# Performance work log

Measured on AMD Instinct MI355X. Metric: run time of the kernel, lower is better.

Reference implementation:

```python
import jax, jax.numpy as jnp
import numpy as np

B, D, H, DH, L = 2, 1024, 16, 64, 4
FF = 4 * D
COUNTS = (512, 256, 128, 64, 16)  # seq, local_seq, scattering, expression, fusion
EPS = 1e-5


def layer_norm(x, gamma):
    mu = jnp.mean(x, axis=-1, keepdims=True)
    var = jnp.mean((x - mu) ** 2, axis=-1, keepdims=True)
    return (x - mu) * jax.lax.rsqrt(var + EPS) * gamma


def build_zorro_mask(counts):
    # faithful to the torch code, including the `|` / `==` precedence quirk:
    # zorro_mask_fusion = (zorro_mask | tf) == FUSION(4)
    types = jnp.concatenate([jnp.full((c,), i, dtype=jnp.int32) for i, c in enumerate(counts)])
    tf, tt = types[:, None], types[None, :]
    m0 = tf == tt
    fusion_rows = (m0.astype(jnp.int32) | tf) == 4
    mask = m0 | fusion_rows
    S = int(sum(counts))
    nf = counts[4]
    exp_rows = (types == 3)[:, None]
    col_ok = (jnp.arange(S) < (S - nf))[None, :]
    return mask | (exp_rows & col_ok)


def setup_inputs() -> dict:
    key = jax.random.key(0)
    ks = jax.random.split(key, 13)
    s = 0.02
    inp = {
        "rna_tokens": jax.random.normal(ks[0], (B, COUNTS[0], D), jnp.float32),
        "roi_tokens": jax.random.normal(ks[1], (B, COUNTS[1], D), jnp.float32),
        "structure_tokens": jax.random.normal(ks[2], (B, COUNTS[2], D), jnp.float32),
        "expression_tokens": jax.random.normal(ks[3], (B, COUNTS[3], D), jnp.float32),
        "fusion_tokens": jax.random.normal(ks[4], (B, COUNTS[4], D), jnp.float32),
        "qw": jax.random.normal(ks[5], (L, D, H * DH), jnp.float32) * s,
        "kvw": jax.random.normal(ks[6], (L, D, 2 * H * DH), jnp.float32) * s,
        "ow": jax.random.normal(ks[7], (L, H * DH, D), jnp.float32) * s,
        "ag": jnp.ones((L, D), jnp.float32),
        "fg": jnp.ones((L, D), jnp.float32),
        "w1": jax.random.normal(ks[8], (L, D, FF), jnp.float32) * s,
        "w2": jax.random.normal(ks[9], (L, FF, D), jnp.float32) * s,
        "gamma": jnp.ones((D,), jnp.float32),
    }
    return inp


def reference(rna_tokens, roi_tokens, structure_tokens, expression_tokens, fusion_tokens,
              qw, kvw, ow, ag, fg, w1, w2, gamma):
    streams = (rna_tokens, roi_tokens, structure_tokens, expression_tokens, fusion_tokens)
    counts = tuple(t.shape[1] for t in streams)
    tokens = jnp.concatenate(streams, axis=1)  # [B, S, D]
    b, S, d = tokens.shape
    mask = build_zorro_mask(counts)  # [S, S] bool
    scale = DH ** -0.5
    neg = jnp.finfo(tokens.dtype).min
    attn_list = []
    for l in range(L):
        x = layer_norm(tokens, ag[l])
        q = (x @ qw[l]).reshape(b, S, H, DH)
        kv = x @ kvw[l]
        k = kv[..., : H * DH].reshape(b, S, H, DH)
        v = kv[..., H * DH:].reshape(b, S, H, DH)
        sim = jnp.einsum('bihd,bjhd->bhij', q, k) * scale
        sim = jnp.where(mask, sim, neg)
        attn = jax.nn.softmax(sim, axis=-1)  # [B, H, S, S]
        attn_list.append(attn)
        out = jnp.einsum('bhij,bjhd->bihd', attn, v).reshape(b, S, H * DH) @ ow[l]
        tokens = out + tokens
        y = layer_norm(tokens, fg[l])
        tokens = jax.nn.gelu(y @ w1[l], approximate=False) @ w2[l] + tokens
    tokens = layer_norm(tokens, gamma)
    splits = np.cumsum(counts)[:-1].tolist()
    seq_t, local_t, scat_t, exp_t, fus_t = jnp.split(tokens, splits, axis=1)
    return (seq_t, local_t, scat_t, exp_t, fus_t, jnp.stack(attn_list))
```

## Files before the change

kernel.cpp:

```cpp
#include <hip/hip_runtime.h>
#include <math.h>
#include <stdint.h>

typedef __bf16 bf16;
typedef __attribute__((ext_vector_type(8))) bf16 bf16x8;
typedef __attribute__((ext_vector_type(4))) bf16 bf16x4;
typedef __attribute__((ext_vector_type(4))) float f4;

__device__ __forceinline__ f4 mfma(bf16x8 a, bf16x8 b, f4 c){
  return __builtin_amdgcn_mfma_f32_16x16x32_bf16(a, b, c, 0, 0, 0);
}

static constexpr int S_TOT = 976;
static constexpr int MR = 1952;
static constexpr int MRP = 2048;
static constexpr size_t ATT_BASE = 1998848;
static constexpr size_t ATT_L = 30482432;

__device__ __forceinline__ void gload16(const void* g, const void* l){
  __builtin_amdgcn_global_load_lds(
      (const __attribute__((address_space(1))) void*)(uintptr_t)g,
      (__attribute__((address_space(3))) void*)(uint32_t)(uintptr_t)l,
      16, 0, 0);
}

__device__ __forceinline__ unsigned pk2(float a, float b){
  unsigned short ua = __builtin_bit_cast(unsigned short, (bf16)a);
  unsigned short ub = __builtin_bit_cast(unsigned short, (bf16)b);
  return ((unsigned)ub << 16) | (unsigned)ua;
}

__global__ __launch_bounds__(256) void k_concat(const float* __restrict__ r0, const float* __restrict__ r1,
                                                const float* __restrict__ r2, const float* __restrict__ r3,
                                                const float* __restrict__ r4, float* __restrict__ tok){
  int idx = blockIdx.x*256 + threadIdx.x;
  if (idx >= MR*256) return;
  int d4 = idx & 255;
  int row = idx >> 8;
  int b = row / S_TOT, s = row % S_TOT;
  const float* src; int off;
  if (s < 512)      { src = r0; off = b*512 + s; }
  else if (s < 768) { src = r1; off = b*256 + (s-512); }
  else if (s < 896) { src = r2; off = b*128 + (s-768); }
  else if (s < 960) { src = r3; off = b*64  + (s-896); }
  else              { src = r4; off = b*16  + (s-960); }
  ((f4*)tok)[idx] = ((const f4*)src)[off*256 + d4];
}

__global__ __launch_bounds__(256) void k_ln_bf(const float* __restrict__ in, const float* __restrict__ g,
                                               bf16* __restrict__ out){
  int wid = threadIdx.x >> 6, lane = threadIdx.x & 63;
  int row = blockIdx.x*4 + wid;
  const float* p = in + (size_t)row*1024;
  f4 v[4];
#pragma unroll
  for (int i=0;i<4;i++) v[i] = ((const f4*)p)[i*64 + lane];
  float sum=0.f, sq=0.f;
#pragma unroll
  for (int i=0;i<4;i++){
#pragma unroll
    for (int c=0;c<4;c++){ float x=v[i][c]; sum+=x; sq+=x*x; } }
#pragma unroll
  for (int d=1; d<64; d<<=1){ sum += __shfl_xor(sum,d); sq += __shfl_xor(sq,d); }
  float mu = sum*(1.f/1024.f);
  float var = sq*(1.f/1024.f) - mu*mu;
  float rs = rsqrtf(var + 1e-5f);
#pragma unroll
  for (int i=0;i<4;i++){
    f4 gg = ((const f4*)g)[i*64 + lane];
    bf16x4 o;
#pragma unroll
    for (int c=0;c<4;c++) o[c] = (bf16)((v[i][c]-mu)*rs*gg[c]);
    *(bf16x4*)&out[(size_t)row*1024 + (size_t)(i*64+lane)*4] = o;
  }
}

__global__ __launch_bounds__(256) void k_ln_out(const float* __restrict__ in, const float* __restrict__ g,
                                                float* __restrict__ out){
  int wid = threadIdx.x >> 6, lane = threadIdx.x & 63;
  int row = blockIdx.x*4 + wid;
  int b = row / S_TOT, s = row % S_TOT;
  size_t dst;
  if (s < 512)      dst = (size_t)(b*512 + s)*1024;
  else if (s < 768) dst = 1048576 + (size_t)(b*256 + (s-512))*1024;
  else if (s < 896) dst = 1572864 + (size_t)(b*128 + (s-768))*1024;
  else if (s < 960) dst = 1835008 + (size_t)(b*64  + (s-896))*1024;
  else              dst = 1966080 + (size_t)(b*16  + (s-960))*1024;
  const float* p = in + (size_t)row*1024;
  f4 v[4];
#pragma unroll
  for (int i=0;i<4;i++) v[i] = ((const f4*)p)[i*64 + lane];
  float sum=0.f, sq=0.f;
#pragma unroll
  for (int i=0;i<4;i++){
#pragma unroll
    for (int c=0;c<4;c++){ float x=v[i][c]; sum+=x; sq+=x*x; } }
#pragma unroll
  for (int d=1; d<64; d<<=1){ sum += __shfl_xor(sum,d); sq += __shfl_xor(sq,d); }
  float mu = sum*(1.f/1024.f);
  float var = sq*(1.f/1024.f) - mu*mu;
  float rs = rsqrtf(var + 1e-5f);
#pragma unroll
  for (int i=0;i<4;i++){
    f4 gg = ((const f4*)g)[i*64 + lane];
    f4 o;
#pragma unroll
    for (int c=0;c<4;c++) o[c] = (v[i][c]-mu)*rs*gg[c];
    ((f4*)(out + dst))[i*64 + lane] = o;
  }
}

__global__ __launch_bounds__(256) void k_wtransz(const float* __restrict__ src, int ldsrc, int coloff, long srcZ,
                                                 bf16* __restrict__ dst, int K, long dstZ){
  src += (size_t)blockIdx.z*srcZ;
  dst += (size_t)blockIdx.z*dstZ;
  __shared__ float t[32][33];
  int kb = blockIdx.x*32, nb = blockIdx.y*32;
  int tx = threadIdx.x & 31, ty = threadIdx.x >> 5;
#pragma unroll
  for (int i=0;i<32;i+=8) t[ty+i][tx] = src[(size_t)(kb+ty+i)*ldsrc + coloff + nb + tx];
  __syncthreads();
#pragma unroll
  for (int i=0;i<32;i+=8) dst[(size_t)(nb+ty+i)*K + kb + tx] = (bf16)t[tx][ty+i];
}

__global__ __launch_bounds__(256) void k_attn_pv(const bf16* __restrict__ q, const bf16* __restrict__ k,
                                                 const bf16* __restrict__ vT, int ld,
                                                 float* __restrict__ aout, bf16* __restrict__ O){
  int z = blockIdx.y; int b = z >> 4, h = z & 15;
  int wid = threadIdx.x >> 6, lane = threadIdx.x & 63;
  int r0 = (blockIdx.x*4 + wid)*16;
  if (r0 >= S_TOT) return;
  int cs, ce;
  if (r0 < 512)      { cs = 0;   ce = 512; }
  else if (r0 < 768) { cs = 512; ce = 768; }
  else if (r0 < 896) { cs = 768; ce = 896; }
  else if (r0 < 960) { cs = 0;   ce = 960; }
  else               { cs = 0;   ce = 976; }
  int lm = lane & 15, lg = lane >> 4;
  const float scale = 0.125f;
  const bf16* qp = q + (size_t)(b*S_TOT + r0 + lm)*ld + h*64 + lg*8;
  bf16x8 qf0 = *(const bf16x8*)qp;
  bf16x8 qf1 = *(const bf16x8*)(qp + 32);
  const bf16* kbase = k + (size_t)b*S_TOT*ld + h*64 + lg*8;
  const bf16* vbase = vT + (size_t)z*64*S_TOT;
  int nfull = (ce - cs) & ~31;
  bool tail = ((ce - cs) & 16) != 0;
  float m = -1e30f, s = 0.f;
  for (int cb = cs; cb < cs + nfull; cb += 32){
    const bf16* kp = kbase + (size_t)(cb + lm)*ld;
    bf16x8 k00 = *(const bf16x8*)kp;
    bf16x8 k01 = *(const bf16x8*)(kp + 32);
    const bf16* kp2 = kp + (size_t)16*ld;
    bf16x8 k10 = *(const bf16x8*)kp2;
    bf16x8 k11 = *(const bf16x8*)(kp2 + 32);
    f4 c0 = {0.f,0.f,0.f,0.f}, c1 = {0.f,0.f,0.f,0.f};
    c0 = mfma(k00, qf0, c0); c0 = mfma(k01, qf1, c0);
    c1 = mfma(k10, qf0, c1); c1 = mfma(k11, qf1, c1);
    float vm = m;
#pragma unroll
    for (int r=0;r<4;r++) vm = fmaxf(vm, fmaxf(c0[r]*scale, c1[r]*scale));
    float e = 0.f;
#pragma unroll
    for (int r=0;r<4;r++) e += __expf(c0[r]*scale - vm) + __expf(c1[r]*scale - vm);
    s = s*__expf(m - vm) + e;
    m = vm;
  }
  if (tail){
    int cb = cs + nfull;
    const bf16* kp = kbase + (size_t)(cb + lm)*ld;
    bf16x8 k00 = *(const bf16x8*)kp;
    bf16x8 k01 = *(const bf16x8*)(kp + 32);
    f4 c0 = {0.f,0.f,0.f,0.f};
    c0 = mfma(k00, qf0, c0); c0 = mfma(k01, qf1, c0);
    float vm = m;
#pragma unroll
    for (int r=0;r<4;r++) vm = fmaxf(vm, c0[r]*scale);
    float e = 0.f;
#pragma unroll
    for (int r=0;r<4;r++) e += __expf(c0[r]*scale - vm);
    s = s*__expf(m - vm) + e;
    m = vm;
  }
#pragma unroll
  for (int d=16; d<64; d<<=1){
    float om = __shfl_xor(m, d), os = __shfl_xor(s, d);
    float nm = fmaxf(m, om);
    s = s*__expf(m - nm) + os*__expf(om - nm);
    m = nm;
  }
  float inv = 1.f / s;
  float* orow = aout + (size_t)z*S_TOT*S_TOT + (size_t)(r0 + lm)*S_TOT;
  f4 acc[4];
#pragma unroll
  for (int nf=0;nf<4;nf++){ f4 zf = {0.f,0.f,0.f,0.f}; acc[nf] = zf; }
  bool msel = (lg >= 2);
  int srcA = lm + ((lg & 1) << 5);
  int srcB = srcA + 16;
  auto step = [&](int cb, bool has2){
    const bf16* kp = kbase + (size_t)(cb + lm)*ld;
    bf16x8 k00 = *(const bf16x8*)kp;
    bf16x8 k01 = *(const bf16x8*)(kp + 32);
    f4 c0 = {0.f,0.f,0.f,0.f}, c1 = {0.f,0.f,0.f,0.f};
    c0 = mfma(k00, qf0, c0); c0 = mfma(k01, qf1, c0);
    if (has2){
      const bf16* kp2 = kp + (size_t)16*ld;
      bf16x8 k10 = *(const bf16x8*)kp2;
      bf16x8 k11 = *(const bf16x8*)(kp2 + 32);
      c1 = mfma(k10, qf0, c1); c1 = mfma(k11, qf1, c1);
    }
    f4 p0, p1;
#pragma unroll
    for (int r=0;r<4;r++) p0[r] = __expf(c0[r]*scale - m)*inv;
#pragma unroll
    for (int r=0;r<4;r++) p1[r] = has2 ? __expf(c1[r]*scale - m)*inv : 0.f;
    *(f4*)(orow + cb + lg*4) = p0;
    if (has2) *(f4*)(orow + cb + 16 + lg*4) = p1;
    unsigned lo0 = pk2(p0[0], p0[1]), hi0 = pk2(p0[2], p0[3]);
    unsigned lo1 = pk2(p1[0], p1[1]), hi1 = pk2(p1[2], p1[3]);
    unsigned a0 = __shfl(lo0, srcA), a1 = __shfl(lo1, srcA);
    unsigned b0 = __shfl(hi0, srcA), b1 = __shfl(hi1, srcA);
    unsigned c0s = __shfl(lo0, srcB), c1s = __shfl(lo1, srcB);
    unsigned d0 = __shfl(hi0, srcB), d1 = __shfl(hi1, srcB);
    union { unsigned u[4]; bf16x8 v; } pu;
    pu.u[0] = msel ? a1 : a0;
    pu.u[1] = msel ? b1 : b0;
    pu.u[2] = msel ? c1s : c0s;
    pu.u[3] = msel ? d1 : d0;
    bf16x8 pa = pu.v;
#pragma unroll
    for (int nf=0;nf<4;nf++){
      bf16x8 vf = *(const bf16x8*)(vbase + (size_t)(nf*16 + lm)*S_TOT + cb + lg*8);
      acc[nf] = mfma(pa, vf, acc[nf]);
    }
  };
  for (int cb = cs; cb < cs + nfull; cb += 32) step(cb, true);
  if (tail) step(cs + nfull, false);
  bf16* obase = O + (size_t)(b*S_TOT + r0)*1024 + h*64;
#pragma unroll
  for (int nf=0;nf<4;nf++)
#pragma unroll
    for (int r=0;r<4;r++)
      obase[(size_t)(lg*4 + r)*1024 + nf*16 + lm] = (bf16)acc[nf][r];
  float* zrow = aout + (size_t)z*S_TOT*S_TOT + (size_t)r0*S_TOT;
  int cs4 = cs >> 2, ce4 = ce >> 2;
  for (int r2=0;r2<16;r2++){
    f4* rb = (f4*)(zrow + (size_t)r2*S_TOT);
    f4 zf = {0.f,0.f,0.f,0.f};
    for (int c4 = lane; c4 < cs4; c4 += 64)        rb[c4] = zf;
    for (int c4 = ce4 + lane; c4 < 244; c4 += 64)  rb[c4] = zf;
  }
}

template<int BM, bool OUTBF, bool RESID, bool GELU, bool VT>
__global__ __launch_bounds__(256) void k_gemm2(
    const bf16* __restrict__ A, int lda,
    const bf16* __restrict__ Bw, int ldb,
    float* __restrict__ Cf, bf16* __restrict__ Cb, int ldc,
    const float* __restrict__ R, bf16* __restrict__ vTout, int M, int N, int K)
{
  constexpr int MF = BM/32;
  __shared__ bf16 As[2][BM*32];
  __shared__ bf16 Bs[2][128*32];
  int tid = threadIdx.x, lane = tid & 63, wid = tid >> 6;
  int lm = lane & 15, lg = lane >> 4;
  int wr = (wid >> 1)*(BM/2), wc = (wid & 1)*64;
  int mb = blockIdx.x*BM, nb = blockIdx.y*128;
  f4 acc[MF][4];
#pragma unroll
  for (int i=0;i<MF;i++)
#pragma unroll
    for (int j=0;j<4;j++){ f4 zf = {0.f,0.f,0.f,0.f}; acc[i][j] = zf; }
  const bf16* Ab = A + (size_t)mb*lda;
  const bf16* Bb = Bw + (size_t)nb*ldb;
  auto stage = [&](int kt, int buf){
    int k0 = kt*32;
#pragma unroll
    for (int it=0; it<BM/64; it++){
      int cb = it*256 + wid*64;
      int c  = cb + lane;
      gload16(Ab + (size_t)(c>>2)*lda + k0 + (c&3)*8, (char*)As[buf] + cb*16);
    }
#pragma unroll
    for (int it=0; it<2; it++){
      int cb = it*256 + wid*64;
      int c  = cb + lane;
      gload16(Bb + (size_t)(c>>2)*ldb + k0 + (c&3)*8, (char*)Bs[buf] + cb*16);
    }
  };
  stage(0, 0);
  __syncthreads();
  int nkt = K/32;
  for (int kt=0; kt<nkt; kt++){
    int cur = kt & 1;
    if (kt+1 < nkt) stage(kt+1, cur^1);
    bf16x8 af[MF], bfr[4];
#pragma unroll
    for (int mf=0; mf<MF; mf++) af[mf] = *(bf16x8*)&As[cur][(wr + mf*16 + lm)*32 + lg*8];
#pragma unroll
    for (int nf=0; nf<4; nf++)  bfr[nf] = *(bf16x8*)&Bs[cur][(wc + nf*16 + lm)*32 + lg*8];
#pragma unroll
    for (int mf=0; mf<MF; mf++)
#pragma unroll
      for (int nf=0; nf<4; nf++)
        acc[mf][nf] = mfma(af[mf], bfr[nf], acc[mf][nf]);
    __syncthreads();
  }
#pragma unroll
  for (int mf=0; mf<MF; mf++)
#pragma unroll
    for (int nf=0; nf<4; nf++)
#pragma unroll
      for (int r=0; r<4; r++){
        int row = mb + wr + mf*16 + lg*4 + r;
        if (row < M){
          int col = nb + wc + nf*16 + lm;
          float vv = acc[mf][nf][r];
          if (RESID) vv += R[(size_t)row*ldc + col];
          if (GELU)  vv = 0.5f*vv*(1.f + erff(vv*0.70710678f));
          if (OUTBF) Cb[(size_t)row*ldc + col] = (bf16)vv;
          else       Cf[(size_t)row*ldc + col] = vv;
          if (VT && nb >= 2048){
            int cc = col - 2048;
            int hh = cc >> 6, dd = cc & 63;
            int bb = (row >= S_TOT) ? 1 : 0;
            int ss = row - bb*S_TOT;
            vTout[((size_t)((bb<<4) + hh)*64 + dd)*S_TOT + ss] = (bf16)vv;
          }
        }
      }
}

extern "C" void kernel_launch(void* const* d_in, const int* in_sizes, int n_in,
                              void* d_out, int out_size, void* d_ws, size_t ws_size,
                              hipStream_t stream) {
  const float* rna  = (const float*)d_in[0];
  const float* roi  = (const float*)d_in[1];
  const float* stru = (const float*)d_in[2];
  const float* expr = (const float*)d_in[3];
  const float* fus  = (const float*)d_in[4];
  const float* qw   = (const float*)d_in[5];
  const float* kvw  = (const float*)d_in[6];
  const float* ow   = (const float*)d_in[7];
  const float* ag   = (const float*)d_in[8];
  const float* fg   = (const float*)d_in[9];
  const float* w1   = (const float*)d_in[10];
  const float* w2   = (const float*)d_in[11];
  const float* gamma= (const float*)d_in[12];
  float* out = (float*)d_out;

  char* wsb = (char*)d_ws;
  size_t off = 0;
  auto alc = [&](size_t n)->char*{ char* p = wsb + off; off = (off + n + 255) & ~(size_t)255; return p; };
  float* tokens = (float*)alc((size_t)MRP*1024*4);
  bf16* xb    = (bf16*)alc((size_t)MRP*1024*2);
  bf16* qkv   = (bf16*)alc((size_t)MRP*3072*2);
  bf16* vT    = (bf16*)alc((size_t)32*64*S_TOT*2);
  bf16* attno = (bf16*)alc((size_t)MRP*1024*2);
  bf16* hb    = (bf16*)alc((size_t)MRP*4096*2);
  bf16* wqkvT = (bf16*)alc((size_t)4*3072*1024*2);
  bf16* woT   = (bf16*)alc((size_t)4*1024*1024*2);
  bf16* w1T   = (bf16*)alc((size_t)4*4096*1024*2);
  bf16* w2T   = (bf16*)alc((size_t)4*4096*1024*2);
  if (off > ws_size) return;

  k_concat<<<MR, 256, 0, stream>>>(rna, roi, stru, expr, fus, tokens);

  k_wtransz<<<dim3(32,32,4),  256, 0, stream>>>(qw,  1024, 0,    1048576, wqkvT,             1024, 3145728);
  k_wtransz<<<dim3(32,32,4),  256, 0, stream>>>(kvw, 2048, 0,    2097152, wqkvT + 1024*1024, 1024, 3145728);
  k_wtransz<<<dim3(32,32,4),  256, 0, stream>>>(kvw, 2048, 1024, 2097152, wqkvT + 2048*1024, 1024, 3145728);
  k_wtransz<<<dim3(32,32,4),  256, 0, stream>>>(ow,  1024, 0,    1048576, woT, 1024, 1048576);
  k_wtransz<<<dim3(32,128,4), 256, 0, stream>>>(w1,  4096, 0,    4194304, w1T, 1024, 4194304);
  k_wtransz<<<dim3(128,32,4), 256, 0, stream>>>(w2,  1024, 0,    4194304, w2T, 4096, 4194304);

  for (int l=0; l<4; l++){
    k_ln_bf<<<MR/4, 256, 0, stream>>>(tokens, ag + l*1024, xb);

    k_gemm2<128,true,false,false,true><<<dim3(16,24), 256, 0, stream>>>(
        xb, 1024, wqkvT + (size_t)l*3145728, 1024, nullptr, qkv, 3072, nullptr, vT, MR, 3072, 1024);

    float* attL = out + ATT_BASE + (size_t)l*ATT_L;
    k_attn_pv<<<dim3(16,32), 256, 0, stream>>>(qkv, qkv + 1024, vT, 3072, attL, attno);

    k_gemm2<64,false,true,false,false><<<dim3(31,8), 256, 0, stream>>>(
        attno, 1024, woT + (size_t)l*1048576, 1024, tokens, nullptr, 1024, tokens, nullptr, MR, 1024, 1024);

    k_ln_bf<<<MR/4, 256, 0, stream>>>(tokens, fg + l*1024, xb);

    k_gemm2<128,true,false,true,false><<<dim3(16,32), 256, 0, stream>>>(
        xb, 1024, w1T + (size_t)l*4194304, 1024, nullptr, hb, 4096, nullptr, nullptr, MR, 4096, 1024);
    k_gemm2<64,false,true,false,false><<<dim3(31,8), 256, 0, stream>>>(
        hb, 4096, w2T + (size_t)l*4194304, 4096, tokens, nullptr, 1024, tokens, nullptr, MR, 1024, 4096);
  }

  k_ln_out<<<MR/4, 256, 0, stream>>>(tokens, gamma, out);
}
```

Measured before the change: 1.184 ms.

## Split-K the FFN down-projection, fuse residual reduction with next LayerNorm, separate V transpose

The FFN down-projection GEMM now splits K=4096 into two halves across blockIdx.z and uses 128-row tiles, writing fp32 partials to a new workspace buffer. A new kernel sums both partials with the residual and, when another layer follows, also computes the next attention LayerNorm, which removes a separate LN launch. The V transpose moves out of the QKV GEMM epilogue into a dedicated LDS-tiled transpose kernel, and s_setprio hints are placed around the MFMA blocks in the attention kernel. The split-K path adds extra fp32 partial traffic and one more launch per layer in exchange for more blocks on the narrow N=1024 GEMM.

```diff
diff --git a/kernel.cpp b/kernel.cpp
--- a/kernel.cpp
+++ b/kernel.cpp
@@ -75,6 +75,42 @@
   }
 }
 
+template<bool LN>
+__global__ __launch_bounds__(256) void k_red_ln(const float* __restrict__ pA, float* __restrict__ tokens,
+                                                const float* __restrict__ g, bf16* __restrict__ xb){
+  int wid = threadIdx.x >> 6, lane = threadIdx.x & 63;
+  int row = blockIdx.x*4 + wid;
+  const float* p0 = pA + (size_t)row*1024;
+  const float* p1 = pA + (size_t)MRP*1024 + (size_t)row*1024;
+  float* tp = tokens + (size_t)row*1024;
+  f4 v[4];
+  float sum=0.f, sq=0.f;
+#pragma unroll
+  for (int i=0;i<4;i++){
+    f4 a = ((const f4*)p0)[i*64 + lane];
+    f4 b = ((const f4*)p1)[i*64 + lane];
+    f4 t = ((const f4*)tp)[i*64 + lane];
+#pragma unroll
+    for (int c=0;c<4;c++){ float x = t[c] + a[c] + b[c]; v[i][c] = x; if (LN){ sum += x; sq += x*x; } }
+    ((f4*)tp)[i*64 + lane] = v[i];
+  }
+  if (LN){
+#pragma unroll
+    for (int d=1; d<64; d<<=1){ sum += __shfl_xor(sum,d); sq += __shfl_xor(sq,d); }
+    float mu = sum*(1.f/1024.f);
+    float var = sq*(1.f/1024.f) - mu*mu;
+    float rs = rsqrtf(var + 1e-5f);
+#pragma unroll
+    for (int i=0;i<4;i++){
+      f4 gg = ((const f4*)g)[i*64 + lane];
+      bf16x4 o;
+#pragma unroll
+      for (int c=0;c<4;c++) o[c] = (bf16)((v[i][c]-mu)*rs*gg[c]);
+      *(bf16x4*)&xb[(size_t)row*1024 + (size_t)(i*64+lane)*4] = o;
+    }
+  }
+}
+
 __global__ __launch_bounds__(256) void k_ln_out(const float* __restrict__ in, const float* __restrict__ g,
                                                 float* __restrict__ out){
   int wid = threadIdx.x >> 6, lane = threadIdx.x & 63;
@@ -122,6 +158,24 @@
   __syncthreads();
 #pragma unroll
   for (int i=0;i<32;i+=8) dst[(size_t)(nb+ty+i)*K + kb + tx] = (bf16)t[tx][ty+i];
+}
+
+__global__ __launch_bounds__(256) void k_vtrans(const bf16* __restrict__ v, int ld, bf16* __restrict__ vT){
+  int z = blockIdx.y; int b = z >> 4, h = z & 15;
+  int sb = blockIdx.x*64;
+  __shared__ bf16 t[64][72];
+  int tx = threadIdx.x & 63, ty = threadIdx.x >> 6;
+#pragma unroll
+  for (int i=0;i<64;i+=4){
+    int s = sb + ty + i;
+    t[ty+i][tx] = (s < S_TOT) ? v[(size_t)(b*S_TOT + s)*ld + h*64 + tx] : (bf16)0.f;
+  }
+  __syncthreads();
+#pragma unroll
+  for (int i=0;i<64;i+=4){
+    int s = sb + tx;
+    if (s < S_TOT) vT[(size_t)z*64*S_TOT + (size_t)(ty+i)*S_TOT + s] = t[tx][ty+i];
+  }
 }
 
 __global__ __launch_bounds__(256) void k_attn_pv(const bf16* __restrict__ q, const bf16* __restrict__ k,
@@ -155,8 +209,10 @@
     bf16x8 k10 = *(const bf16x8*)kp2;
     bf16x8 k11 = *(const bf16x8*)(kp2 + 32);
     f4 c0 = {0.f,0.f,0.f,0.f}, c1 = {0.f,0.f,0.f,0.f};
+    __builtin_amdgcn_s_setprio(1);
     c0 = mfma(k00, qf0, c0); c0 = mfma(k01, qf1, c0);
     c1 = mfma(k10, qf0, c1); c1 = mfma(k11, qf1, c1);
+    __builtin_amdgcn_s_setprio(0);
     float vm = m;
 #pragma unroll
     for (int r=0;r<4;r++) vm = fmaxf(vm, fmaxf(c0[r]*scale, c1[r]*scale));
@@ -202,6 +258,7 @@
     bf16x8 k00 = *(const bf16x8*)kp;
     bf16x8 k01 = *(const bf16x8*)(kp + 32);
     f4 c0 = {0.f,0.f,0.f,0.f}, c1 = {0.f,0.f,0.f,0.f};
+    __builtin_amdgcn_s_setprio(1);
     c0 = mfma(k00, qf0, c0); c0 = mfma(k01, qf1, c0);
     if (has2){
       const bf16* kp2 = kp + (size_t)16*ld;
@@ -209,6 +266,7 @@
       bf16x8 k11 = *(const bf16x8*)(kp2 + 32);
       c1 = mfma(k10, qf0, c1); c1 = mfma(k11, qf1, c1);
     }
+    __builtin_amdgcn_s_setprio(0);
     f4 p0, p1;
 #pragma unroll
     for (int r=0;r<4;r++) p0[r] = __expf(c0[r]*scale - m)*inv;
@@ -228,11 +286,13 @@
     pu.u[2] = msel ? c1s : c0s;
     pu.u[3] = msel ? d1 : d0;
     bf16x8 pa = pu.v;
+    __builtin_amdgcn_s_setprio(1);
 #pragma unroll
     for (int nf=0;nf<4;nf++){
       bf16x8 vf = *(const bf16x8*)(vbase + (size_t)(nf*16 + lm)*S_TOT + cb + lg*8);
       acc[nf] = mfma(pa, vf, acc[nf]);
     }
+    __builtin_amdgcn_s_setprio(0);
   };
   for (int cb = cs; cb < cs + nfull; cb += 32) step(cb, true);
   if (tail) step(cs + nfull, false);
@@ -252,12 +312,12 @@
   }
 }
 
-template<int BM, bool OUTBF, bool RESID, bool GELU, bool VT>
+template<int BM, bool OUTBF, bool RESID, bool GELU>
 __global__ __launch_bounds__(256) void k_gemm2(
     const bf16* __restrict__ A, int lda,
     const bf16* __restrict__ Bw, int ldb,
     float* __restrict__ Cf, bf16* __restrict__ Cb, int ldc,
-    const float* __restrict__ R, bf16* __restrict__ vTout, int M, int N, int K)
+    const float* __restrict__ R, int M, int N, int K, int kz, long cz)
 {
   constexpr int MF = BM/32;
   __shared__ bf16 As[2][BM*32];
@@ -266,13 +326,14 @@
   int lm = lane & 15, lg = lane >> 4;
   int wr = (wid >> 1)*(BM/2), wc = (wid & 1)*64;
   int mb = blockIdx.x*BM, nb = blockIdx.y*128;
+  int bz = blockIdx.z;
   f4 acc[MF][4];
 #pragma unroll
   for (int i=0;i<MF;i++)
 #pragma unroll
     for (int j=0;j<4;j++){ f4 zf = {0.f,0.f,0.f,0.f}; acc[i][j] = zf; }
-  const bf16* Ab = A + (size_t)mb*lda;
-  const bf16* Bb = Bw + (size_t)nb*ldb;
+  const bf16* Ab = A + (size_t)mb*lda + (size_t)bz*kz;
+  const bf16* Bb = Bw + (size_t)nb*ldb + (size_t)bz*kz;
   auto stage = [&](int kt, int buf){
     int k0 = kt*32;
 #pragma unroll
@@ -319,14 +380,7 @@
           if (RESID) vv += R[(size_t)row*ldc + col];
           if (GELU)  vv = 0.5f*vv*(1.f + erff(vv*0.70710678f));
           if (OUTBF) Cb[(size_t)row*ldc + col] = (bf16)vv;
-          else       Cf[(size_t)row*ldc + col] = vv;
-          if (VT && nb >= 2048){
-            int cc = col - 2048;
-            int hh = cc >> 6, dd = cc & 63;
-            int bb = (row >= S_TOT) ? 1 : 0;
-            int ss = row - bb*S_TOT;
-            vTout[((size_t)((bb<<4) + hh)*64 + dd)*S_TOT + ss] = (bf16)vv;
-          }
+          else       Cf[(size_t)bz*cz + (size_t)row*ldc + col] = vv;
         }
       }
 }
@@ -353,6 +407,7 @@
   size_t off = 0;
   auto alc = [&](size_t n)->char*{ char* p = wsb + off; off = (off + n + 255) & ~(size_t)255; return p; };
   float* tokens = (float*)alc((size_t)MRP*1024*4);
+  float* pA    = (float*)alc((size_t)2*MRP*1024*4);
   bf16* xb    = (bf16*)alc((size_t)MRP*1024*2);
   bf16* qkv   = (bf16*)alc((size_t)MRP*3072*2);
   bf16* vT    = (bf16*)alc((size_t)32*64*S_TOT*2);
@@ -373,24 +428,31 @@
   k_wtransz<<<dim3(32,128,4), 256, 0, stream>>>(w1,  4096, 0,    4194304, w1T, 1024, 4194304);
   k_wtransz<<<dim3(128,32,4), 256, 0, stream>>>(w2,  1024, 0,    4194304, w2T, 4096, 4194304);
 
+  k_ln_bf<<<MR/4, 256, 0, stream>>>(tokens, ag, xb);
+
   for (int l=0; l<4; l++){
-    k_ln_bf<<<MR/4, 256, 0, stream>>>(tokens, ag + l*1024, xb);
-
-    k_gemm2<128,true,false,false,true><<<dim3(16,24), 256, 0, stream>>>(
-        xb, 1024, wqkvT + (size_t)l*3145728, 1024, nullptr, qkv, 3072, nullptr, vT, MR, 3072, 1024);
+    k_gemm2<128,true,false,false><<<dim3(16,24), 256, 0, stream>>>(
+        xb, 1024, wqkvT + (size_t)l*3145728, 1024, nullptr, qkv, 3072, nullptr, MR, 3072, 1024, 0, 0);
+
+    k_vtrans<<<dim3(16,32), 256, 0, stream>>>(qkv + 2048, 3072, vT);
 
     float* attL = out + ATT_BASE + (size_t)l*ATT_L;
     k_attn_pv<<<dim3(16,32), 256, 0, stream>>>(qkv, qkv + 1024, vT, 3072, attL, attno);
 
-    k_gemm2<64,false,true,false,false><<<dim3(31,8), 256, 0, stream>>>(
-        attno, 1024, woT + (size_t)l*1048576, 1024, tokens, nullptr, 1024, tokens, nullptr, MR, 1024, 1024);
+    k_gemm2<64,false,true,false><<<dim3(31,8), 256, 0, stream>>>(
+        attno, 1024, woT + (size_t)l*1048576, 1024, tokens, nullptr, 1024, tokens, MR, 1024, 1024, 0, 0);
 
     k_ln_bf<<<MR/4, 256, 0, stream>>>(tokens, fg + l*1024, xb);
 
-    k_gemm2<128,true,false,true,false><<<dim3(16,32), 256, 0, stream>>>(
-        xb, 1024, w1T + (size_t)l*4194304, 1024, nullptr, hb, 4096, nullptr, nullptr, MR, 4096, 1024);
-    k_gemm2<64,false,true,false,false><<<dim3(31,8), 256, 0, stream>>>(
-        hb, 4096, w2T + (size_t)l*4194304, 4096, tokens, nullptr, 1024, tokens, nullptr, MR, 1024, 4096);
+    k_gemm2<128,true,false,true><<<dim3(16,32), 256, 0, stream>>>(
+        xb, 1024, w1T + (size_t)l*4194304, 1024, nullptr, hb, 4096, nullptr, MR, 4096, 1024, 0, 0);
+
+    k_gemm2<128,false,false,false><<<dim3(16,8,2), 256, 0, stream>>>(
+        hb, 4096, w2T + (size_t)l*4194304, 4096, pA, nullptr, 1024, nullptr, MR, 1024, 2048,
+        2048, (long)MRP*1024);
+
+    if (l < 3) k_red_ln<true><<<MR/4, 256, 0, stream>>>(pA, tokens, ag + (l+1)*1024, xb);
+    else       k_red_ln<false><<<MR/4, 256, 0, stream>>>(pA, tokens, nullptr, nullptr);
   }
 
   k_ln_out<<<MR/4, 256, 0, stream>>>(tokens, gamma, out);
```

Result: faster. 1.067 ms (-9.9%).
